# Optimization experiments

Hardware: AMD Instinct MI355X
Metric: run time of the kernel (lower is better)

Reference implementation:

```python
import jax, jax.numpy as jnp
import numpy as np

B, T, P, Z, H, K = 2048, 256, 5, 128, 1024, 20
O = 6 * K + 3  # 123


def setup_inputs() -> dict:
    key = jax.random.key(0)
    ks = jax.random.split(key, 10)
    def lin(k, shape, fan_in):
        return jax.random.normal(k, shape, dtype=jnp.float32) / np.sqrt(fan_in)
    return {
        "s": jax.random.normal(ks[0], (B, T, P), dtype=jnp.float32),
        "z": jax.random.normal(ks[1], (B, Z), dtype=jnp.float32),
        "w_h0": lin(ks[2], (H, Z), Z),
        "b_h0": jnp.zeros((H,), jnp.float32),
        "w_ih": lin(ks[3], (4 * H, P + Z), P + Z),
        "b_ih": jnp.zeros((4 * H,), jnp.float32),
        "w_hh": lin(ks[4], (4 * H, H), H),
        "b_hh": jnp.zeros((4 * H,), jnp.float32),
        "w_dec": lin(ks[5], (O, H), H),
        "b_dec": jnp.zeros((O,), jnp.float32),
    }


def reference(s, z, w_h0, b_h0, w_ih, b_ih, w_hh, b_hh, w_dec, b_dec):
    batch = s.shape[0]
    # initial decoder state: h0 = tanh(fc_h0(z)), c0 = 0
    h0 = jnp.tanh(z @ w_h0.T + b_h0)
    c0 = jnp.zeros((batch, H), s.dtype)
    # input point sequence: step 0 uses the start token, step i uses s[:, i-1]
    s0 = jnp.broadcast_to(jnp.array([0.0, 0.0, 1.0, 0.0, 0.0], s.dtype), (batch, P))
    seq = jnp.concatenate([s0[None], jnp.swapaxes(s, 0, 1)[: T - 1]], axis=0)  # [T,B,5]

    def step(carry, s_i):
        h, c = carry
        x = jnp.concatenate([s_i, z], axis=1)  # [B, 133]
        gates = x @ w_ih.T + b_ih + h @ w_hh.T + b_hh  # [B, 4H]
        i_g, f_g, g_g, o_g = jnp.split(gates, 4, axis=1)
        c_new = jax.nn.sigmoid(f_g) * c + jax.nn.sigmoid(i_g) * jnp.tanh(g_g)
        h_new = jax.nn.sigmoid(o_g) * jnp.tanh(c_new)
        y = h_new @ w_dec.T + b_dec  # [B, 123]
        mix = y[:, : 6 * K].reshape(batch, K, 6)  # interleaved per-mixture params
        t_pi = jax.nn.softmax(mix[:, :, 0], axis=1)
        t_mean1 = mix[:, :, 1]
        t_mean2 = mix[:, :, 2]
        t_std_x = jnp.exp(mix[:, :, 3])
        t_std_y = jnp.exp(mix[:, :, 4])
        t_cor = jnp.tanh(mix[:, :, 5])
        # NOTE: original normalizes qk by the sum over the ENTIRE batch (torch.sum
        # with no dim) -- faithfully reproduced.
        exp_qk = jnp.exp(y[:, 6 * K :])
        t_qk = exp_qk / jnp.sum(exp_qk)
        out = jnp.concatenate(
            [t_pi, t_mean1, t_mean2, t_std_x, t_std_y, t_cor, t_qk], axis=1
        )  # [B, 123]
        return (h_new, c_new), out

    _, outs = jax.lax.scan(step, (h0, c0), seq)  # outs: [T, B, 123]
    output = jnp.swapaxes(outs, 0, 1)  # [B, T, 123]
    mu = jnp.zeros((Z,), s.dtype)
    presig = jnp.zeros((Z,), s.dtype)
    return output, mu, presig
```

## Files before the change

### kernel.cpp

```cpp
#include <hip/hip_runtime.h>

using bf16x8 = __attribute__((ext_vector_type(8))) __bf16;
using f32x4  = __attribute__((ext_vector_type(4))) float;
typedef unsigned short ushort_t;

constexpr int NB = 2048;
constexpr int NT = 256;
constexpr int NP = 5;
constexpr int NZ = 128;
constexpr int NH = 1024;
constexpr int NK = 20;
constexpr int NO = 123;
constexpr int TO_ = NT * NO;

constexpr size_t HBUF_OFF = 0;
constexpr size_t WHH_OFF  = 8ull  * 1024 * 1024;
constexpr size_t WZ_OFF   = 16ull * 1024 * 1024;
constexpr size_t WDEC_OFF = 17ull * 1024 * 1024;
constexpr size_t ZBF_OFF  = 17ull * 1024 * 1024 + 512 * 1024;
constexpr size_t YWS_OFF  = 18ull * 1024 * 1024;
constexpr size_t CWS_OFF  = 19ull * 1024 * 1024;
constexpr size_t QK_OFF   = 27ull * 1024 * 1024;

__device__ __forceinline__ ushort_t f2bfr(float f) {
  unsigned int v; __builtin_memcpy(&v, &f, 4);
  v += 0x7fffu + ((v >> 16) & 1u);
  return (ushort_t)(v >> 16);
}
__device__ __forceinline__ float sigm(float x) { return 1.f / (1.f + __expf(-x)); }
__device__ __forceinline__ float tanh_(float x) {
  x = fminf(fmaxf(x, -30.f), 30.f);
  float e = __expf(2.f * x);
  return (e - 1.f) / (e + 1.f);
}
__device__ __forceinline__ float wredmax(float v) {
  #pragma unroll
  for (int m = 32; m; m >>= 1) v = fmaxf(v, __shfl_xor(v, m, 64));
  return v;
}
__device__ __forceinline__ float wredsum(float v) {
  #pragma unroll
  for (int m = 32; m; m >>= 1) v += __shfl_xor(v, m, 64);
  return v;
}

__device__ __forceinline__ void gload16(const void* g, void* l) {
  __builtin_amdgcn_global_load_lds(
      (const __attribute__((address_space(1))) void*)g,
      (__attribute__((address_space(3))) void*)l, 16, 0, 0);
}

__device__ __forceinline__ void do_transform(const float* __restrict__ yrow, float qkt,
                                             float* __restrict__ outp, int lane) {
  float pv = (lane < NK) ? yrow[lane * 6] : -3.0e38f;
  float mx = wredmax(pv);
  float ev = (lane < NK) ? __expf(pv - mx) : 0.f;
  float sm = wredsum(ev);
  if (lane < NK) {
    outp[lane]          = ev / sm;
    outp[NK + lane]     = yrow[lane * 6 + 1];
    outp[2 * NK + lane] = yrow[lane * 6 + 2];
    outp[3 * NK + lane] = __expf(fminf(yrow[lane * 6 + 3], 80.f));
    outp[4 * NK + lane] = __expf(fminf(yrow[lane * 6 + 4], 80.f));
    outp[5 * NK + lane] = tanh_(yrow[lane * 6 + 5]);
  }
  if (lane < 3)
    outp[6 * NK + lane] = __expf(fminf(yrow[120 + lane], 80.f)) / qkt;
}

__global__ __launch_bounds__(512)
void prep_kernel(const float* __restrict__ whh, const float* __restrict__ wih,
                 const float* __restrict__ wdec, const float* __restrict__ zIn,
                 ushort_t* __restrict__ whh_bf, ushort_t* __restrict__ wz_bf,
                 ushort_t* __restrict__ wdec_bf, ushort_t* __restrict__ z_bf) {
  const int stride = 256 * 512;
  const int t0 = blockIdx.x * 512 + threadIdx.x;
  for (int i = t0; i < 4096 * 1024; i += stride) whh_bf[i] = f2bfr(whh[i]);
  for (int i = t0; i < 4096 * 128; i += stride) {
    int g = i >> 7, k = i & 127;
    wz_bf[i] = f2bfr(wih[(size_t)g * (NP + NZ) + NP + k]);
  }
  for (int i = t0; i < 123 * 1024; i += stride) wdec_bf[i] = f2bfr(wdec[i]);
  for (int i = t0; i < 2048 * 128;  i += stride) z_bf[i]  = f2bfr(zIn[i]);
}

__global__ __launch_bounds__(512)
void h0_kernel(const float* __restrict__ zIn, const float* __restrict__ wh0,
               const float* __restrict__ bh0, ushort_t* __restrict__ hout) {
  const int tid = threadIdx.x, blk = blockIdx.x;
  const int b0 = (blk >> 4) * 128, h0c = (blk & 15) * 64;
  const int m = tid >> 2, jg = tid & 3;
  const float* zr = zIn + (size_t)(b0 + m) * NZ;
  for (int j = jg * 16; j < jg * 16 + 16; ++j) {
    int hcol = h0c + j;
    float a = bh0[hcol];
    const float* wr = wh0 + (size_t)hcol * NZ;
    for (int q = 0; q < NZ; ++q) a += zr[q] * wr[q];
    hout[(size_t)(b0 + m) * NH + hcol] = f2bfr(tanh_(a));
  }
}

__global__ __launch_bounds__(256, 2)
void stepA_kernel(int t,
                  const float* __restrict__ sIn, const ushort_t* __restrict__ z_bf,
                  const float* __restrict__ wih, const float* __restrict__ bih,
                  const float* __restrict__ bhh,
                  const ushort_t* __restrict__ whh_bf, const ushort_t* __restrict__ wz_bf,
                  const ushort_t* __restrict__ hin, ushort_t* __restrict__ hout,
                  float* __restrict__ cws, const float* __restrict__ yws,
                  const float* __restrict__ qks, float* __restrict__ out) {
  __shared__ __attribute__((aligned(16))) ushort_t aLds[2][128 * 64];
  __shared__ __attribute__((aligned(16))) ushort_t bLds[2][128 * 64];
  __shared__ float wPl[128 * NP];
  __shared__ float bl[128];
  __shared__ float sPl[128 * NP];

  const int tid = threadIdx.x, blk = blockIdx.x;
  const int wave = tid >> 6, lane = tid & 63;
  const int wm = wave & 1, wn = wave >> 1;
  const int l15 = lane & 15, l4 = lane >> 4;
  const int b_grp = blk >> 5, h_grp = blk & 31;
  const int b0 = b_grp * 128, h0c = h_grp * 32;

  const int lr     = lane >> 3;
  const int lclog  = (lane & 7) ^ lr;

  auto stageA = [&](int buf, int kt) {
    #pragma unroll
    for (int j = 0; j < 4; ++j) {
      int ch = wave * 4 + j;
      int r = ch * 8 + lr;
      const ushort_t* src = (kt < 16)
        ? &hin[(size_t)(b0 + r) * NH + kt * 64 + lclog * 8]
        : &z_bf[(size_t)(b0 + r) * NZ + (kt - 16) * 64 + lclog * 8];
      gload16(src, &aLds[buf][ch * 512]);
    }
  };
  auto stageB = [&](int buf, int kt) {
    #pragma unroll
    for (int j = 0; j < 4; ++j) {
      int ch = wave * 4 + j;
      int rn = ch * 8 + lr;
      int grow = (rn >> 5) * NH + h0c + (rn & 31);
      const ushort_t* src = (kt < 16)
        ? &whh_bf[(size_t)grow * NH + kt * 64 + lclog * 8]
        : &wz_bf[(size_t)grow * 128 + (kt - 16) * 64 + lclog * 8];
      gload16(src, &bLds[buf][ch * 512]);
    }
  };

  stageA(0, 0); stageB(0, 0);

  if (t > 0) {
    int b = blk * 4 + wave;
    float qkt = __hip_atomic_load(&qks[t - 1], __ATOMIC_RELAXED, __HIP_MEMORY_SCOPE_AGENT);
    do_transform(yws + (size_t)b * 128, qkt,
                 out + (size_t)b * TO_ + (size_t)(t - 1) * NO, lane);
  }

  for (int idx = tid; idx < 128 * NP; idx += 256) {
    int rn = idx / NP, p = idx - rn * NP;
    int grow = (rn >> 5) * NH + h0c + (rn & 31);
    wPl[idx] = wih[(size_t)grow * (NP + NZ) + p];
  }
  if (tid < 128) {
    int grow = (tid >> 5) * NH + h0c + (tid & 31);
    bl[tid] = bih[grow] + bhh[grow];
  }
  for (int idx = tid; idx < 128 * NP; idx += 256) {
    int r = idx / NP, p = idx - r * NP;
    float v;
    if (t == 0) v = (p == 2) ? 1.f : 0.f;
    else        v = sIn[(size_t)(b0 + r) * (NT * NP) + (size_t)(t - 1) * NP + p];
    sPl[idx] = v;
  }

  f32x4 acc[4][4];
  #pragma unroll
  for (int mi = 0; mi < 4; ++mi)
    #pragma unroll
    for (int s = 0; s < 4; ++s) acc[mi][s] = f32x4{0.f, 0.f, 0.f, 0.f};

  __syncthreads();

  for (int kt = 0; kt < 18; ++kt) {
    const int cur = kt & 1;
    if (kt < 17) {
      stageA(cur ^ 1, kt + 1); stageB(cur ^ 1, kt + 1);
      asm volatile("s_waitcnt vmcnt(8)" ::: "memory");
    } else {
      asm volatile("s_waitcnt vmcnt(0)" ::: "memory");
    }
    __builtin_amdgcn_s_barrier();
    asm volatile("" ::: "memory");
    #pragma unroll
    for (int kk = 0; kk < 2; ++kk) {
      bf16x8 af[4], bfg[4];
      #pragma unroll
      for (int mi = 0; mi < 4; ++mi) {
        int r = wm * 64 + mi * 16 + l15;
        af[mi] = *(const bf16x8*)&aLds[cur][r * 64 + (((kk * 4 + l4) ^ (l15 & 7)) * 8)];
      }
      #pragma unroll
      for (int s = 0; s < 4; ++s) {
        int rn = s * 32 + wn * 16 + l15;
        bfg[s] = *(const bf16x8*)&bLds[cur][rn * 64 + (((kk * 4 + l4) ^ (l15 & 7)) * 8)];
      }
      __builtin_amdgcn_s_setprio(1);
      #pragma unroll
      for (int mi = 0; mi < 4; ++mi)
        #pragma unroll
        for (int s = 0; s < 4; ++s)
          acc[mi][s] = __builtin_amdgcn_mfma_f32_16x16x32_bf16(af[mi], bfg[s], acc[mi][s], 0, 0, 0);
      __builtin_amdgcn_s_setprio(0);
    }
    asm volatile("" ::: "memory");
    __builtin_amdgcn_s_barrier();
    asm volatile("" ::: "memory");
  }

  float wpv[4][NP];
  #pragma unroll
  for (int s = 0; s < 4; ++s) {
    int nl = s * 32 + wn * 16 + l15;
    #pragma unroll
    for (int p = 0; p < NP; ++p) wpv[s][p] = wPl[nl * NP + p];
  }
  const int colh = h0c + wn * 16 + l15;
  #pragma unroll
  for (int mi = 0; mi < 4; ++mi) {
    #pragma unroll
    for (int e = 0; e < 4; ++e) {
      int m = wm * 64 + mi * 16 + l4 * 4 + e;
      float sv0 = sPl[m * NP + 0], sv1 = sPl[m * NP + 1], sv2 = sPl[m * NP + 2];
      float sv3 = sPl[m * NP + 3], sv4 = sPl[m * NP + 4];
      float gv[4];
      #pragma unroll
      for (int s = 0; s < 4; ++s) {
        int nl = s * 32 + wn * 16 + l15;
        gv[s] = acc[mi][s][e] + bl[nl]
              + sv0 * wpv[s][0] + sv1 * wpv[s][1] + sv2 * wpv[s][2]
              + sv3 * wpv[s][3] + sv4 * wpv[s][4];
      }
      float ig = sigm(gv[0]);
      float fg = sigm(gv[1]);
      float gg = tanh_(gv[2]);
      float og = sigm(gv[3]);
      size_t ci = (size_t)(b0 + m) * NH + colh;
      float cn = fg * cws[ci] + ig * gg;
      cws[ci] = cn;
      hout[ci] = f2bfr(og * tanh_(cn));
    }
  }
}

__global__ __launch_bounds__(256)
void stepB_kernel(int t, const ushort_t* __restrict__ hcur,
                  const ushort_t* __restrict__ wdec_bf, const float* __restrict__ bdec,
                  float* __restrict__ yws, float* __restrict__ qks) {
  __shared__ __attribute__((aligned(16))) ushort_t hLds[16 * 1032];
  const int tid = threadIdx.x, blk = blockIdx.x;
  const int wave = tid >> 6, lane = tid & 63;
  const int l15 = lane & 15, l4 = lane >> 4;
  const int r0 = (blk >> 1) * 16;
  const int chalf = blk & 1;

  #pragma unroll
  for (int j = 0; j < 8; ++j) {
    int id = tid + 256 * j;
    int r = id >> 7, c = id & 127;
    *(uint4*)&hLds[r * 1032 + c * 8] = *(const uint4*)&hcur[(size_t)(r0 + r) * NH + c * 8];
  }
  __syncthreads();

  const int col = chalf * 64 + wave * 16 + l15;
  const int brow = col > 122 ? 122 : col;
  const ushort_t* ha = &hLds[l15 * 1032 + l4 * 8];
  const ushort_t* wb = wdec_bf + (size_t)brow * NH + l4 * 8;
  f32x4 dacc = {0.f, 0.f, 0.f, 0.f};
  #pragma unroll 8
  for (int k2 = 0; k2 < 32; ++k2) {
    bf16x8 a = *(const bf16x8*)(ha + k2 * 32);
    bf16x8 b = *(const bf16x8*)(wb + k2 * 32);
    dacc = __builtin_amdgcn_mfma_f32_16x16x32_bf16(a, b, dacc, 0, 0, 0);
  }
  float bd = (col < NO) ? bdec[col] : 0.f;
  #pragma unroll
  for (int e = 0; e < 4; ++e)
    yws[(size_t)(r0 + l4 * 4 + e) * 128 + col] = dacc[e] + bd;

  if (chalf == 1 && wave == 3) {
    float qp = 0.f;
    if (l15 >= 8 && l15 <= 10) {
      #pragma unroll
      for (int e = 0; e < 4; ++e) qp += __expf(fminf(dacc[e] + bd, 80.f));
    }
    qp = wredsum(qp);
    if (lane == 0) atomicAdd(&qks[t], qp);
  }
}

__global__ __launch_bounds__(512)
void finalC_kernel(const float* __restrict__ yws, const float* __restrict__ qks,
                   float* __restrict__ out) {
  const int tid = threadIdx.x, blk = blockIdx.x;
  const int wave = tid >> 6, lane = tid & 63;
  int b = blk * 8 + wave;
  float qkt = __hip_atomic_load(&qks[NT - 1], __ATOMIC_RELAXED, __HIP_MEMORY_SCOPE_AGENT);
  do_transform(yws + (size_t)b * 128, qkt,
               out + (size_t)b * TO_ + (size_t)(NT - 1) * NO, lane);
  if (blk == 0 && tid < 2 * NZ)
    out[(size_t)NB * TO_ + tid] = 0.f;
}

extern "C" void kernel_launch(void* const* d_in, const int* in_sizes, int n_in,
                              void* d_out, int out_size, void* d_ws, size_t ws_size,
                              hipStream_t stream) {
  const float* sIn  = (const float*)d_in[0];
  const float* zIn  = (const float*)d_in[1];
  const float* wh0  = (const float*)d_in[2];
  const float* bh0  = (const float*)d_in[3];
  const float* wih  = (const float*)d_in[4];
  const float* bih  = (const float*)d_in[5];
  const float* whh  = (const float*)d_in[6];
  const float* bhh  = (const float*)d_in[7];
  const float* wdec = (const float*)d_in[8];
  const float* bdec = (const float*)d_in[9];
  float* out = (float*)d_out;
  char* ws = (char*)d_ws;
  ushort_t* hbuf    = (ushort_t*)(ws + HBUF_OFF);
  ushort_t* whh_bf  = (ushort_t*)(ws + WHH_OFF);
  ushort_t* wz_bf   = (ushort_t*)(ws + WZ_OFF);
  ushort_t* wdec_bf = (ushort_t*)(ws + WDEC_OFF);
  ushort_t* z_bf    = (ushort_t*)(ws + ZBF_OFF);
  float*    yws     = (float*)(ws + YWS_OFF);
  float*    cws     = (float*)(ws + CWS_OFF);
  float*    qks     = (float*)(ws + QK_OFF);

  hipMemsetAsync(cws, 0, (size_t)NB * NH * 4, stream);
  hipMemsetAsync(qks, 0, NT * 4, stream);
  prep_kernel<<<256, 512, 0, stream>>>(whh, wih, wdec, zIn, whh_bf, wz_bf, wdec_bf, z_bf);
  h0_kernel<<<256, 512, 0, stream>>>(zIn, wh0, bh0, hbuf + (size_t)NB * NH);

  for (int t = 0; t < NT; ++t) {
    const ushort_t* hin = hbuf + (size_t)((t + 1) & 1) * NB * NH;
    ushort_t*      hout = hbuf + (size_t)(t & 1) * NB * NH;
    stepA_kernel<<<512, 256, 0, stream>>>(t, sIn, z_bf, wih, bih, bhh, whh_bf, wz_bf,
                                          hin, hout, cws, yws, qks, out);
    stepB_kernel<<<256, 256, 0, stream>>>(t, hout, wdec_bf, bdec, yws, qks);
  }
  finalC_kernel<<<256, 512, 0, stream>>>(yws, qks, out);
}
```

Before: 10.78 ms.

## Fuse decoder GEMM into next LSTM step kernel, deferring output transform by one step

The decoder projection y = h_t·W_decᵀ for step t-1 is now computed inside the step-t gate GEMM kernel, reusing the h tiles already staged in LDS. A subset of blocks loads W_dec tiles and issues extra MFMAs. This removes the separate per-step decoder kernel launch and its re-read of h. The y workspace is double-buffered and the output transform lags two steps, with the tail handled after the loop. The K-loop is also restructured to a single-wait, single-barrier double buffer with precomputed pointers, which adds load imbalance across blocks because only some of them do decoder work.

```diff
diff --git a/kernel.cpp b/kernel.cpp
--- a/kernel.cpp
+++ b/kernel.cpp
@@ -19,8 +19,8 @@
 constexpr size_t WDEC_OFF = 17ull * 1024 * 1024;
 constexpr size_t ZBF_OFF  = 17ull * 1024 * 1024 + 512 * 1024;
 constexpr size_t YWS_OFF  = 18ull * 1024 * 1024;
-constexpr size_t CWS_OFF  = 19ull * 1024 * 1024;
-constexpr size_t QK_OFF   = 27ull * 1024 * 1024;
+constexpr size_t CWS_OFF  = 20ull * 1024 * 1024;
+constexpr size_t QK_OFF   = 28ull * 1024 * 1024;
 
 __device__ __forceinline__ ushort_t f2bfr(float f) {
   unsigned int v; __builtin_memcpy(&v, &f, 4);
@@ -106,11 +106,14 @@
                   const float* __restrict__ wih, const float* __restrict__ bih,
                   const float* __restrict__ bhh,
                   const ushort_t* __restrict__ whh_bf, const ushort_t* __restrict__ wz_bf,
+                  const ushort_t* __restrict__ wdec_bf, const float* __restrict__ bdec,
                   const ushort_t* __restrict__ hin, ushort_t* __restrict__ hout,
-                  float* __restrict__ cws, const float* __restrict__ yws,
-                  const float* __restrict__ qks, float* __restrict__ out) {
+                  float* __restrict__ cws, const float* __restrict__ yws_r,
+                  float* __restrict__ yws_w, float* __restrict__ qks,
+                  float* __restrict__ out) {
   __shared__ __attribute__((aligned(16))) ushort_t aLds[2][128 * 64];
   __shared__ __attribute__((aligned(16))) ushort_t bLds[2][128 * 64];
+  __shared__ __attribute__((aligned(16))) ushort_t dLds[2][16 * 64];
   __shared__ float wPl[128 * NP];
   __shared__ float bl[128];
   __shared__ float sPl[128 * NP];
@@ -121,41 +124,49 @@
   const int l15 = lane & 15, l4 = lane >> 4;
   const int b_grp = blk >> 5, h_grp = blk & 31;
   const int b0 = b_grp * 128, h0c = h_grp * 32;
-
-  const int lr     = lane >> 3;
-  const int lclog  = (lane & 7) ^ lr;
-
-  auto stageA = [&](int buf, int kt) {
+  const bool DECB = (h_grp < 8) && (t > 0);
+  const int dcol0 = h_grp * 16;
+
+  const int lr    = lane >> 3;
+  const int lclog = (lane & 7) ^ lr;
+
+  const ushort_t* pA[4]; const ushort_t* pB[4];
+  #pragma unroll
+  for (int j = 0; j < 4; ++j) {
+    int r = wave * 32 + j * 8 + lr;
+    pA[j] = hin + (size_t)(b0 + r) * NH + lclog * 8;
+    int grow = (r >> 5) * NH + h0c + (r & 31);
+    pB[j] = whh_bf + (size_t)grow * NH + lclog * 8;
+  }
+  const ushort_t* pD = wdec_bf + (size_t)(dcol0 + wave * 8 + lr) * NH + lclog * 8;
+
+  auto stage_h = [&](int buf) {
     #pragma unroll
     for (int j = 0; j < 4; ++j) {
-      int ch = wave * 4 + j;
-      int r = ch * 8 + lr;
-      const ushort_t* src = (kt < 16)
-        ? &hin[(size_t)(b0 + r) * NH + kt * 64 + lclog * 8]
-        : &z_bf[(size_t)(b0 + r) * NZ + (kt - 16) * 64 + lclog * 8];
-      gload16(src, &aLds[buf][ch * 512]);
-    }
+      gload16(pA[j], &aLds[buf][(wave * 4 + j) * 512]);  pA[j] += 64;
+      gload16(pB[j], &bLds[buf][(wave * 4 + j) * 512]);  pB[j] += 64;
+    }
+    if (DECB && wave < 2) { gload16(pD, &dLds[buf][wave * 512]); pD += 64; }
   };
-  auto stageB = [&](int buf, int kt) {
+  auto stage_z = [&](int buf, int zi) {
     #pragma unroll
     for (int j = 0; j < 4; ++j) {
-      int ch = wave * 4 + j;
-      int rn = ch * 8 + lr;
-      int grow = (rn >> 5) * NH + h0c + (rn & 31);
-      const ushort_t* src = (kt < 16)
-        ? &whh_bf[(size_t)grow * NH + kt * 64 + lclog * 8]
-        : &wz_bf[(size_t)grow * 128 + (kt - 16) * 64 + lclog * 8];
-      gload16(src, &bLds[buf][ch * 512]);
+      int r = wave * 32 + j * 8 + lr;
+      gload16(z_bf + (size_t)(b0 + r) * NZ + zi * 64 + lclog * 8,
+              &aLds[buf][(wave * 4 + j) * 512]);
+      int grow = (r >> 5) * NH + h0c + (r & 31);
+      gload16(wz_bf + (size_t)grow * 128 + zi * 64 + lclog * 8,
+              &bLds[buf][(wave * 4 + j) * 512]);
     }
   };
 
-  stageA(0, 0); stageB(0, 0);
-
-  if (t > 0) {
+  stage_h(0);
+
+  if (t > 1) {
     int b = blk * 4 + wave;
-    float qkt = __hip_atomic_load(&qks[t - 1], __ATOMIC_RELAXED, __HIP_MEMORY_SCOPE_AGENT);
-    do_transform(yws + (size_t)b * 128, qkt,
-                 out + (size_t)b * TO_ + (size_t)(t - 1) * NO, lane);
+    float qkt = __hip_atomic_load(&qks[t - 2], __ATOMIC_RELAXED, __HIP_MEMORY_SCOPE_AGENT);
+    do_transform(yws_r + (size_t)b * 128, qkt,
+                 out + (size_t)b * TO_ + (size_t)(t - 2) * NO, lane);
   }
 
   for (int idx = tid; idx < 128 * NP; idx += 256) {
@@ -180,43 +191,67 @@
   for (int mi = 0; mi < 4; ++mi)
     #pragma unroll
     for (int s = 0; s < 4; ++s) acc[mi][s] = f32x4{0.f, 0.f, 0.f, 0.f};
+  f32x4 dacc[2] = {f32x4{0.f, 0.f, 0.f, 0.f}, f32x4{0.f, 0.f, 0.f, 0.f}};
+
+  const int q8a = (l4 ^ (l15 & 7)) * 8;
+  const int q8b = ((4 + l4) ^ (l15 & 7)) * 8;
 
   __syncthreads();
 
   for (int kt = 0; kt < 18; ++kt) {
     const int cur = kt & 1;
-    if (kt < 17) {
-      stageA(cur ^ 1, kt + 1); stageB(cur ^ 1, kt + 1);
-      asm volatile("s_waitcnt vmcnt(8)" ::: "memory");
-    } else {
+    if (kt) {
       asm volatile("s_waitcnt vmcnt(0)" ::: "memory");
-    }
-    __builtin_amdgcn_s_barrier();
-    asm volatile("" ::: "memory");
+      __builtin_amdgcn_s_barrier();
+    }
+    if (kt < 15)      stage_h(cur ^ 1);
+    else if (kt < 17) stage_z(cur ^ 1, kt - 15);
+    const bool dk = DECB && (kt < 16);
     #pragma unroll
     for (int kk = 0; kk < 2; ++kk) {
-      bf16x8 af[4], bfg[4];
-      #pragma unroll
-      for (int mi = 0; mi < 4; ++mi) {
-        int r = wm * 64 + mi * 16 + l15;
-        af[mi] = *(const bf16x8*)&aLds[cur][r * 64 + (((kk * 4 + l4) ^ (l15 & 7)) * 8)];
-      }
-      #pragma unroll
-      for (int s = 0; s < 4; ++s) {
-        int rn = s * 32 + wn * 16 + l15;
-        bfg[s] = *(const bf16x8*)&bLds[cur][rn * 64 + (((kk * 4 + l4) ^ (l15 & 7)) * 8)];
-      }
+      const int q8 = kk ? q8b : q8a;
+      bf16x8 af[4], bfg[4], df;
+      #pragma unroll
+      for (int mi = 0; mi < 4; ++mi)
+        af[mi] = *(const bf16x8*)&aLds[cur][(wm * 64 + mi * 16 + l15) * 64 + q8];
+      #pragma unroll
+      for (int s = 0; s < 4; ++s)
+        bfg[s] = *(const bf16x8*)&bLds[cur][(s * 32 + wn * 16 + l15) * 64 + q8];
+      if (dk) df = *(const bf16x8*)&dLds[cur][l15 * 64 + q8];
       __builtin_amdgcn_s_setprio(1);
       #pragma unroll
       for (int mi = 0; mi < 4; ++mi)
         #pragma unroll
         for (int s = 0; s < 4; ++s)
           acc[mi][s] = __builtin_amdgcn_mfma_f32_16x16x32_bf16(af[mi], bfg[s], acc[mi][s], 0, 0, 0);
+      if (dk) {
+        dacc[0] = __builtin_amdgcn_mfma_f32_16x16x32_bf16(af[wn * 2 + 0], df, dacc[0], 0, 0, 0);
+        dacc[1] = __builtin_amdgcn_mfma_f32_16x16x32_bf16(af[wn * 2 + 1], df, dacc[1], 0, 0, 0);
+      }
       __builtin_amdgcn_s_setprio(0);
     }
-    asm volatile("" ::: "memory");
-    __builtin_amdgcn_s_barrier();
-    asm volatile("" ::: "memory");
+  }
+
+  if (DECB) {
+    float qp = 0.f;
+    const int dc = dcol0 + l15;
+    const float bd = (dc < NO) ? bdec[dc] : 0.f;
+    #pragma unroll
+    for (int i = 0; i < 2; ++i) {
+      int dmi = wn * 2 + i;
+      #pragma unroll
+      for (int e = 0; e < 4; ++e) {
+        int m = wm * 64 + dmi * 16 + l4 * 4 + e;
+        float yv = dacc[i][e] + bd;
+        yws_w[(size_t)(b0 + m) * 128 + dc] = yv;
+        if (h_grp == 7 && l15 >= 8 && l15 <= 10)
+          qp += __expf(fminf(yv, 80.f));
+      }
+    }
+    if (h_grp == 7) {
+      qp = wredsum(qp);
+      if (lane == 0) atomicAdd(&qks[t - 1], qp);
+    }
   }
 
   float wpv[4][NP];
@@ -306,8 +341,11 @@
   const int tid = threadIdx.x, blk = blockIdx.x;
   const int wave = tid >> 6, lane = tid & 63;
   int b = blk * 8 + wave;
-  float qkt = __hip_atomic_load(&qks[NT - 1], __ATOMIC_RELAXED, __HIP_MEMORY_SCOPE_AGENT);
-  do_transform(yws + (size_t)b * 128, qkt,
+  float q254 = __hip_atomic_load(&qks[NT - 2], __ATOMIC_RELAXED, __HIP_MEMORY_SCOPE_AGENT);
+  do_transform(yws + (size_t)b * 128, q254,
+               out + (size_t)b * TO_ + (size_t)(NT - 2) * NO, lane);
+  float q255 = __hip_atomic_load(&qks[NT - 1], __ATOMIC_RELAXED, __HIP_MEMORY_SCOPE_AGENT);
+  do_transform(yws + (size_t)(NB + b) * 128, q255,
                out + (size_t)b * TO_ + (size_t)(NT - 1) * NO, lane);
   if (blk == 0 && tid < 2 * NZ)
     out[(size_t)NB * TO_ + tid] = 0.f;
@@ -346,8 +384,12 @@
     const ushort_t* hin = hbuf + (size_t)((t + 1) & 1) * NB * NH;
     ushort_t*      hout = hbuf + (size_t)(t & 1) * NB * NH;
     stepA_kernel<<<512, 256, 0, stream>>>(t, sIn, z_bf, wih, bih, bhh, whh_bf, wz_bf,
-                                          hin, hout, cws, yws, qks, out);
-    stepB_kernel<<<256, 256, 0, stream>>>(t, hout, wdec_bf, bdec, yws, qks);
-  }
+                                          wdec_bf, bdec, hin, hout, cws,
+                                          yws + (size_t)(t & 1) * NB * 128,
+                                          yws + (size_t)((t + 1) & 1) * NB * 128,
+                                          qks, out);
+  }
+  stepB_kernel<<<256, 256, 0, stream>>>(NT - 1, hbuf + (size_t)((NT - 1) & 1) * NB * NH,
+                                        wdec_bf, bdec, yws + (size_t)NB * 128, qks);
   finalC_kernel<<<256, 512, 0, stream>>>(yws, qks, out);
 }
```

After: 37.05 ms. 3.44x slower.
